# Performance work log

Measured on AMD Instinct MI355X. Metric: run time of the kernel, lower is better.

The kernel has to match this reference:

```python
import jax, jax.numpy as jnp
import numpy as np

IOU_THRESHOLD = 0.2


def setup_inputs() -> dict:
    key = jax.random.key(0)
    k1, k2, k3 = jax.random.split(key, 3)
    S, Q, X, Y, Z = 3, 64, 128, 128, 32
    C = 21  # 20 semantic classes + no-object
    voxel_logits = jax.random.normal(k1, (S, Q, X, Y, Z), dtype=jnp.float32)
    query_logits = jax.random.normal(k2, (S, 1, Q, C), dtype=jnp.float32)
    sem_prob_dense = jax.random.uniform(k3, (C, X, Y, Z), dtype=jnp.float32)
    return {"voxel_logits": voxel_logits, "query_logits": query_logits,
            "sem_prob_dense": sem_prob_dense}


def reference(voxel_logits, query_logits, sem_prob_dense):
    # voxel_logits: [S, Q, X, Y, Z], query_logits: [S, B, Q, C],
    # sem_prob_dense: [C_sem, X, Y, Z]
    S, Q, X, Y, Z = voxel_logits.shape
    N = X * Y * Z
    voxel_probs = jax.nn.sigmoid(voxel_logits).reshape(S, Q, N)   # MinkowskiSigmoid
    query_probs = jax.nn.softmax(query_logits, axis=-1)           # [S, B, Q, C]

    anchor_v = voxel_probs[0]   # [Q, N]
    anchor_q = query_probs[0]   # [B, Q, C]
    ious = []
    for i in range(1, S):  # small fixed loop over subnets
        aux_v = voxel_probs[i]
        # hard masks for IoU matching (find_matching_indices_v2)
        ma = (anchor_v > 0.5).astype(jnp.float32)  # [Q, N]
        mb = (aux_v > 0.5).astype(jnp.float32)     # [Q, N]
        inter = jnp.einsum('qn,pn->qp', ma, mb)    # [Q, Q]
        union = ma.sum(1)[:, None] + mb.sum(1)[None, :] - inter
        iou = inter / jnp.maximum(union, 1.0)
        aux_idx = jnp.argmax(iou, axis=1)          # best aux query per anchor
        iou_a = jnp.max(iou, axis=1)               # [Q]
        matched = iou_a > IOU_THRESHOLD
        # running-average merge of matched queries, weight i : 1
        merged_q = (anchor_q * i + query_probs[i][:, aux_idx, :]) / (i + 1)
        anchor_q = jnp.where(matched[None, :, None], merged_q, anchor_q)
        merged_v = (anchor_v * i + aux_v[aux_idx]) / (i + 1)
        anchor_v = jnp.where(matched[:, None], merged_v, anchor_v)
        ious.append(iou_a)

    iou_mean = jnp.stack(ious, axis=0).mean(0)     # [Q]
    keep = (iou_mean > IOU_THRESHOLD).astype(anchor_v.dtype)
    # mask out voxels whose ensemble semantic class is empty (class 0)
    sem_class = jnp.argmax(sem_prob_dense, axis=0)           # [X, Y, Z]
    occ = (sem_class != 0).astype(anchor_v.dtype).reshape(N)
    out = anchor_v * keep[:, None] * occ[None, :]
    return out.reshape(Q, X, Y, Z)
```

## Files before the change

kernel.cpp:

```cpp
#include <hip/hip_runtime.h>
#include <math.h>

#define NVOX 524288
#define WPR  8192
#define QN   64
#define SN   3
#define CN   21

__device__ __forceinline__ float sigmoidf_(float x) {
    return 1.0f / (1.0f + expf(-x));
}

__global__ __launch_bounds__(256) void mask_kernel(
    const float* __restrict__ logits, unsigned long long* __restrict__ B) {
    int tid = threadIdx.x;
    int wave = tid >> 6, lane = tid & 63;
    int wbase = (blockIdx.x * 4 + wave) * 4;
#pragma unroll
    for (int k = 0; k < 4; ++k) {
        int wi = wbase + k;
        int r = wi >> 13;
        int w = wi & (WPR - 1);
        float x = logits[r * NVOX + (w << 6) + lane];
        unsigned long long m = __ballot(x > 0.0f);
        if (lane == 0) B[wi] = m;
    }
}

__global__ __launch_bounds__(256) void rowsum_kernel(
    const unsigned long long* __restrict__ B, unsigned int* __restrict__ cnt) {
    int r = blockIdx.x, tid = threadIdx.x;
    const unsigned long long* row = B + r * WPR;
    int s = 0;
    for (int w = tid; w < WPR; w += 256) s += __popcll(row[w]);
    for (int off = 32; off; off >>= 1) s += __shfl_down(s, off);
    __shared__ int red[4];
    if ((tid & 63) == 0) red[tid >> 6] = s;
    __syncthreads();
    if (tid == 0) cnt[r] = (unsigned)(red[0] + red[1] + red[2] + red[3]);
}

__global__ __launch_bounds__(256) void inter_kernel(
    const unsigned long long* __restrict__ Ba,
    const unsigned long long* __restrict__ Bb,
    unsigned int* __restrict__ inter) {
    int q0 = blockIdx.y * 4, p0 = blockIdx.x * 4;
    int tid = threadIdx.x;
    int acc[4][4] = {};
    for (int w = tid; w < WPR; w += 256) {
        unsigned long long a[4], b[4];
#pragma unroll
        for (int i = 0; i < 4; ++i) a[i] = Ba[(q0 + i) * WPR + w];
#pragma unroll
        for (int j = 0; j < 4; ++j) b[j] = Bb[(p0 + j) * WPR + w];
#pragma unroll
        for (int i = 0; i < 4; ++i)
#pragma unroll
            for (int j = 0; j < 4; ++j) acc[i][j] += __popcll(a[i] & b[j]);
    }
    __shared__ int red[16][4];
    int lane = tid & 63, wave = tid >> 6;
#pragma unroll
    for (int i = 0; i < 4; ++i)
#pragma unroll
        for (int j = 0; j < 4; ++j) {
            int v = acc[i][j];
            for (int off = 32; off; off >>= 1) v += __shfl_down(v, off);
            if (lane == 0) red[i * 4 + j][wave] = v;
        }
    __syncthreads();
    if (tid < 16) {
        int s = red[tid][0] + red[tid][1] + red[tid][2] + red[tid][3];
        inter[(q0 + (tid >> 2)) * QN + (p0 + (tid & 3))] = (unsigned)s;
    }
}

__global__ void finalize_kernel(
    const unsigned int* __restrict__ inter,
    const unsigned int* __restrict__ cnt_a,
    const unsigned int* __restrict__ cnt_b,
    int* __restrict__ idx, int* __restrict__ matched,
    float* __restrict__ iou_out,
    int stage2, const float* __restrict__ iou_prev, float* __restrict__ keep) {
    int q = threadIdx.x;
    if (q >= QN) return;
    float na = (float)cnt_a[q];
    float best = -1.0f;
    int bidx = 0;
    for (int p = 0; p < QN; ++p) {
        float fi = (float)inter[q * QN + p];
        float un = fmaxf(na + (float)cnt_b[p] - fi, 1.0f);
        float iou = fi / un;
        if (iou > best) { best = iou; bidx = p; }
    }
    idx[q] = bidx;
    iou_out[q] = best;
    matched[q] = (best > 0.2f) ? 1 : 0;
    if (stage2) keep[q] = (((iou_prev[q] + best) * 0.5f) > 0.2f) ? 1.0f : 0.0f;
}

__global__ __launch_bounds__(256) void mask2_kernel(
    const float* __restrict__ logits,
    const int* __restrict__ idx1, const int* __restrict__ m1,
    unsigned long long* __restrict__ B0p) {
    int tid = threadIdx.x;
    int wave = tid >> 6, lane = tid & 63;
    int wbase = (blockIdx.x * 4 + wave) * 4;
    int q = wbase >> 13;
    int m = m1[q], j = idx1[q];
    const float* L0 = logits;
    const float* L1 = logits + QN * NVOX;
#pragma unroll
    for (int k = 0; k < 4; ++k) {
        int wi = wbase + k;
        int w = wi & (WPR - 1);
        int n = (w << 6) + lane;
        float x0 = L0[q * NVOX + n];
        bool pred;
        if (m) {
            float s0 = sigmoidf_(x0);
            float s1 = sigmoidf_(L1[j * NVOX + n]);
            pred = (s0 + s1) > 1.0f;
        } else {
            pred = x0 > 0.0f;
        }
        unsigned long long mk = __ballot(pred);
        if (lane == 0) B0p[wi] = mk;
    }
}

__global__ __launch_bounds__(256) void final_kernel(
    const float* __restrict__ logits,
    const float* __restrict__ sem,
    const int* __restrict__ idx1_, const int* __restrict__ m1_,
    const int* __restrict__ idx2_, const int* __restrict__ m2_,
    const float* __restrict__ keep_,
    float* __restrict__ out) {
    __shared__ int sidx1[QN], sm1[QN], sidx2[QN], sm2[QN];
    __shared__ float skeep[QN];
    int tid = threadIdx.x;
    if (tid < QN) {
        sidx1[tid] = idx1_[tid]; sm1[tid] = m1_[tid];
        sidx2[tid] = idx2_[tid]; sm2[tid] = m2_[tid];
        skeep[tid] = keep_[tid];
    }
    __syncthreads();
    int n = blockIdx.x * 256 + tid;
    float s0c = sem[n];
    float mx = sem[NVOX + n];
#pragma unroll
    for (int c = 2; c < CN; ++c) mx = fmaxf(mx, sem[c * NVOX + n]);
    float occ = (mx > s0c) ? 1.0f : 0.0f;
    const float* L0 = logits;
    const float* L1 = logits + QN * NVOX;
    const float* L2 = logits + 2 * QN * NVOX;
    for (int q = 0; q < QN; ++q) {
        float a = sigmoidf_(L0[q * NVOX + n]);
        if (sm1[q]) {
            float s1 = sigmoidf_(L1[sidx1[q] * NVOX + n]);
            a = (a + s1) * 0.5f;
        }
        if (sm2[q]) {
            float s2 = sigmoidf_(L2[sidx2[q] * NVOX + n]);
            a = (a * 2.0f + s2) / 3.0f;
        }
        out[q * NVOX + n] = a * skeep[q] * occ;
    }
}

extern "C" void kernel_launch(void* const* d_in, const int* in_sizes, int n_in,
                              void* d_out, int out_size, void* d_ws, size_t ws_size,
                              hipStream_t stream) {
    const float* vox = (const float*)d_in[0];
    const float* sem = (const float*)d_in[2];
    float* out = (float*)d_out;

    char* p = (char*)d_ws;
    unsigned long long* Ball = (unsigned long long*)p;
    unsigned long long* B0  = Ball;
    unsigned long long* B1  = Ball + 1 * QN * WPR;
    unsigned long long* B2  = Ball + 2 * QN * WPR;
    unsigned long long* B0p = Ball + 3 * QN * WPR;
    unsigned int* inter1 = (unsigned int*)(p + 16u * 1024u * 1024u);
    unsigned int* inter2 = inter1 + QN * QN;
    unsigned int* cnt    = inter2 + QN * QN;
    int*   idx1 = (int*)(cnt + 256);
    int*   idx2 = idx1 + QN;
    int*   m1   = idx2 + QN;
    int*   m2   = m1 + QN;
    float* iou1 = (float*)(m2 + QN);
    float* iou2 = iou1 + QN;
    float* keep = iou2 + QN;
    (void)in_sizes; (void)n_in; (void)out_size; (void)ws_size;

    mask_kernel<<<(SN * QN * WPR) / 16, 256, 0, stream>>>(vox, Ball);
    rowsum_kernel<<<SN * QN, 256, 0, stream>>>(Ball, cnt);

    inter_kernel<<<dim3(16, 16), 256, 0, stream>>>(B0, B1, inter1);
    finalize_kernel<<<1, 64, 0, stream>>>(inter1, cnt, cnt + QN, idx1, m1, iou1,
                                          0, nullptr, nullptr);

    mask2_kernel<<<(QN * WPR) / 16, 256, 0, stream>>>(vox, idx1, m1, B0p);
    rowsum_kernel<<<QN, 256, 0, stream>>>(B0p, cnt + 3 * QN);
    inter_kernel<<<dim3(16, 16), 256, 0, stream>>>(B0p, B2, inter2);
    finalize_kernel<<<1, 64, 0, stream>>>(inter2, cnt + 3 * QN, cnt + 2 * QN,
                                          idx2, m2, iou2, 1, iou1, keep);

    final_kernel<<<NVOX / 256, 256, 0, stream>>>(vox, sem, idx1, m1, idx2, m2,
                                                 keep, out);
}
```

Measured before the change: 892.2 us.

## Vectorize all passes with float4, fuse mask+rowsum, precompute occupancy, skip unmatched rows

Rewrites most kernels around float4 loads. The bitmask pass now also produces per-block popcount partials, which removes the separate rowsum kernels. The second-stage mask kernel skips unmatched queries by reusing the stage-0 bitmask in place, and it uses the logit-sum sign test instead of two sigmoids. Occupancy is computed once into a workspace buffer rather than per final block. The final kernel splits queries across two grid rows and uses fast exp and reciprocal intrinsics. The fast sigmoid slightly changes numerics, and the bit layout within each 256-voxel segment is permuted consistently for all masks.

```diff
diff --git a/kernel.cpp b/kernel.cpp
--- a/kernel.cpp
+++ b/kernel.cpp
@@ -1,62 +1,87 @@
 #include <hip/hip_runtime.h>
-#include <math.h>
 
 #define NVOX 524288
+#define NV4  131072
 #define WPR  8192
 #define QN   64
 #define SN   3
 #define CN   21
 
-__device__ __forceinline__ float sigmoidf_(float x) {
-    return 1.0f / (1.0f + expf(-x));
-}
-
-__global__ __launch_bounds__(256) void mask_kernel(
-    const float* __restrict__ logits, unsigned long long* __restrict__ B) {
-    int tid = threadIdx.x;
-    int wave = tid >> 6, lane = tid & 63;
-    int wbase = (blockIdx.x * 4 + wave) * 4;
-#pragma unroll
-    for (int k = 0; k < 4; ++k) {
-        int wi = wbase + k;
-        int r = wi >> 13;
-        int w = wi & (WPR - 1);
-        float x = logits[r * NVOX + (w << 6) + lane];
-        unsigned long long m = __ballot(x > 0.0f);
-        if (lane == 0) B[wi] = m;
-    }
-}
-
-__global__ __launch_bounds__(256) void rowsum_kernel(
-    const unsigned long long* __restrict__ B, unsigned int* __restrict__ cnt) {
-    int r = blockIdx.x, tid = threadIdx.x;
-    const unsigned long long* row = B + r * WPR;
-    int s = 0;
-    for (int w = tid; w < WPR; w += 256) s += __popcll(row[w]);
-    for (int off = 32; off; off >>= 1) s += __shfl_down(s, off);
+typedef unsigned long long u64;
+
+__device__ __forceinline__ float fast_sigmoid(float x) {
+    return __builtin_amdgcn_rcpf(1.0f + __expf(-x));
+}
+
+__global__ __launch_bounds__(256) void mask_rowsum_kernel(
+    const float4* __restrict__ logits4, u64* __restrict__ B,
+    unsigned int* __restrict__ part) {
+    int r = blockIdx.x >> 3, c = blockIdx.x & 7;
+    int tid = threadIdx.x, lane = tid & 63, wave = tid >> 6;
+    const float4* row = logits4 + (size_t)r * NV4;
+    int base = c * (NV4 / 8);
+    int pcnt = 0;
+#pragma unroll 2
+    for (int it = 0; it < 64; ++it) {
+        int idx = base + it * 256 + tid;
+        float4 v = row[idx];
+        int nib = (v.x > 0.f ? 1 : 0) | (v.y > 0.f ? 2 : 0) |
+                  (v.z > 0.f ? 4 : 0) | (v.w > 0.f ? 8 : 0);
+        pcnt += __popc(nib);
+        u64 b0 = __ballot(nib & 1);
+        u64 b1 = __ballot(nib & 2);
+        u64 b2 = __ballot(nib & 4);
+        u64 b3 = __ballot(nib & 8);
+        if (lane == 0) {
+            int seg = idx >> 6;
+            ulonglong2* dst = (ulonglong2*)&B[(size_t)r * WPR + (size_t)seg * 4];
+            dst[0] = make_ulonglong2(b0, b1);
+            dst[1] = make_ulonglong2(b2, b3);
+        }
+    }
+    for (int off = 32; off; off >>= 1) pcnt += __shfl_down(pcnt, off);
     __shared__ int red[4];
-    if ((tid & 63) == 0) red[tid >> 6] = s;
-    __syncthreads();
-    if (tid == 0) cnt[r] = (unsigned)(red[0] + red[1] + red[2] + red[3]);
+    if (lane == 0) red[wave] = pcnt;
+    __syncthreads();
+    if (tid == 0) part[blockIdx.x] = (unsigned)(red[0] + red[1] + red[2] + red[3]);
+}
+
+__global__ __launch_bounds__(256) void occ_kernel(
+    const float4* __restrict__ sem4, float4* __restrict__ occ4) {
+    int n4 = blockIdx.x * 256 + threadIdx.x;
+    float4 s0 = sem4[n4];
+    float4 mx = sem4[NV4 + n4];
+#pragma unroll
+    for (int c = 2; c < CN; ++c) {
+        float4 s = sem4[(size_t)c * NV4 + n4];
+        mx.x = fmaxf(mx.x, s.x); mx.y = fmaxf(mx.y, s.y);
+        mx.z = fmaxf(mx.z, s.z); mx.w = fmaxf(mx.w, s.w);
+    }
+    float4 o;
+    o.x = (mx.x > s0.x) ? 1.f : 0.f; o.y = (mx.y > s0.y) ? 1.f : 0.f;
+    o.z = (mx.z > s0.z) ? 1.f : 0.f; o.w = (mx.w > s0.w) ? 1.f : 0.f;
+    occ4[n4] = o;
 }
 
 __global__ __launch_bounds__(256) void inter_kernel(
-    const unsigned long long* __restrict__ Ba,
-    const unsigned long long* __restrict__ Bb,
+    const u64* __restrict__ Ba, const u64* __restrict__ Bb,
     unsigned int* __restrict__ inter) {
     int q0 = blockIdx.y * 4, p0 = blockIdx.x * 4;
     int tid = threadIdx.x;
+    const ulonglong2* A2 = (const ulonglong2*)Ba;
+    const ulonglong2* B2 = (const ulonglong2*)Bb;
     int acc[4][4] = {};
-    for (int w = tid; w < WPR; w += 256) {
-        unsigned long long a[4], b[4];
-#pragma unroll
-        for (int i = 0; i < 4; ++i) a[i] = Ba[(q0 + i) * WPR + w];
-#pragma unroll
-        for (int j = 0; j < 4; ++j) b[j] = Bb[(p0 + j) * WPR + w];
+    for (int w = tid; w < WPR / 2; w += 256) {
+        ulonglong2 a[4], b[4];
+#pragma unroll
+        for (int i = 0; i < 4; ++i) a[i] = A2[(size_t)(q0 + i) * (WPR / 2) + w];
+#pragma unroll
+        for (int j = 0; j < 4; ++j) b[j] = B2[(size_t)(p0 + j) * (WPR / 2) + w];
 #pragma unroll
         for (int i = 0; i < 4; ++i)
 #pragma unroll
-            for (int j = 0; j < 4; ++j) acc[i][j] += __popcll(a[i] & b[j]);
+            for (int j = 0; j < 4; ++j)
+                acc[i][j] += __popcll(a[i].x & b[j].x) + __popcll(a[i].y & b[j].y);
     }
     __shared__ int red[16][4];
     int lane = tid & 63, wave = tid >> 6;
@@ -77,19 +102,28 @@
 
 __global__ void finalize_kernel(
     const unsigned int* __restrict__ inter,
-    const unsigned int* __restrict__ cnt_a,
-    const unsigned int* __restrict__ cnt_b,
-    int* __restrict__ idx, int* __restrict__ matched,
-    float* __restrict__ iou_out,
+    const unsigned int* __restrict__ pa,
+    const unsigned int* __restrict__ pa_alt, const int* __restrict__ sel,
+    const unsigned int* __restrict__ pb,
+    int* __restrict__ idx, int* __restrict__ matched, float* __restrict__ iou_out,
     int stage2, const float* __restrict__ iou_prev, float* __restrict__ keep) {
+    __shared__ float nb[QN];
     int q = threadIdx.x;
-    if (q >= QN) return;
-    float na = (float)cnt_a[q];
+    unsigned sb = 0;
+#pragma unroll
+    for (int k = 0; k < 8; ++k) sb += pb[q * 8 + k];
+    nb[q] = (float)sb;
+    __syncthreads();
+    const unsigned int* pr = (sel && !sel[q]) ? pa_alt : pa;
+    unsigned sa = 0;
+#pragma unroll
+    for (int k = 0; k < 8; ++k) sa += pr[q * 8 + k];
+    float na = (float)sa;
     float best = -1.0f;
     int bidx = 0;
     for (int p = 0; p < QN; ++p) {
         float fi = (float)inter[q * QN + p];
-        float un = fmaxf(na + (float)cnt_b[p] - fi, 1.0f);
+        float un = fmaxf(na + nb[p] - fi, 1.0f);
         float iou = fi / un;
         if (iou > best) { best = iou; bidx = p; }
     }
@@ -100,112 +134,131 @@
 }
 
 __global__ __launch_bounds__(256) void mask2_kernel(
-    const float* __restrict__ logits,
+    const float4* __restrict__ logits4,
     const int* __restrict__ idx1, const int* __restrict__ m1,
-    unsigned long long* __restrict__ B0p) {
-    int tid = threadIdx.x;
-    int wave = tid >> 6, lane = tid & 63;
-    int wbase = (blockIdx.x * 4 + wave) * 4;
-    int q = wbase >> 13;
-    int m = m1[q], j = idx1[q];
-    const float* L0 = logits;
-    const float* L1 = logits + QN * NVOX;
-#pragma unroll
-    for (int k = 0; k < 4; ++k) {
-        int wi = wbase + k;
-        int w = wi & (WPR - 1);
-        int n = (w << 6) + lane;
-        float x0 = L0[q * NVOX + n];
-        bool pred;
-        if (m) {
-            float s0 = sigmoidf_(x0);
-            float s1 = sigmoidf_(L1[j * NVOX + n]);
-            pred = (s0 + s1) > 1.0f;
-        } else {
-            pred = x0 > 0.0f;
-        }
-        unsigned long long mk = __ballot(pred);
-        if (lane == 0) B0p[wi] = mk;
-    }
+    u64* __restrict__ B0p, unsigned int* __restrict__ partP) {
+    int q = blockIdx.x >> 3, c = blockIdx.x & 7;
+    if (!m1[q]) return;
+    int tid = threadIdx.x, lane = tid & 63, wave = tid >> 6;
+    const float4* r0 = logits4 + (size_t)q * NV4;
+    const float4* r1 = logits4 + (size_t)(QN + idx1[q]) * NV4;
+    int base = c * (NV4 / 8);
+    int pcnt = 0;
+#pragma unroll 2
+    for (int it = 0; it < 64; ++it) {
+        int idx = base + it * 256 + tid;
+        float4 a = r0[idx];
+        float4 b = r1[idx];
+        int nib = (a.x + b.x > 0.f ? 1 : 0) | (a.y + b.y > 0.f ? 2 : 0) |
+                  (a.z + b.z > 0.f ? 4 : 0) | (a.w + b.w > 0.f ? 8 : 0);
+        pcnt += __popc(nib);
+        u64 b0 = __ballot(nib & 1);
+        u64 b1 = __ballot(nib & 2);
+        u64 b2 = __ballot(nib & 4);
+        u64 b3 = __ballot(nib & 8);
+        if (lane == 0) {
+            int seg = idx >> 6;
+            ulonglong2* dst = (ulonglong2*)&B0p[(size_t)q * WPR + (size_t)seg * 4];
+            dst[0] = make_ulonglong2(b0, b1);
+            dst[1] = make_ulonglong2(b2, b3);
+        }
+    }
+    for (int off = 32; off; off >>= 1) pcnt += __shfl_down(pcnt, off);
+    __shared__ int red[4];
+    if (lane == 0) red[wave] = pcnt;
+    __syncthreads();
+    if (tid == 0) partP[blockIdx.x] = (unsigned)(red[0] + red[1] + red[2] + red[3]);
 }
 
 __global__ __launch_bounds__(256) void final_kernel(
-    const float* __restrict__ logits,
-    const float* __restrict__ sem,
+    const float4* __restrict__ logits4, const float4* __restrict__ occ4,
     const int* __restrict__ idx1_, const int* __restrict__ m1_,
     const int* __restrict__ idx2_, const int* __restrict__ m2_,
-    const float* __restrict__ keep_,
-    float* __restrict__ out) {
-    __shared__ int sidx1[QN], sm1[QN], sidx2[QN], sm2[QN];
-    __shared__ float skeep[QN];
+    const float* __restrict__ keep_, float4* __restrict__ out4) {
+    __shared__ int sj1[32], sm1[32], sj2[32], sm2[32];
+    __shared__ float sk[32];
     int tid = threadIdx.x;
-    if (tid < QN) {
-        sidx1[tid] = idx1_[tid]; sm1[tid] = m1_[tid];
-        sidx2[tid] = idx2_[tid]; sm2[tid] = m2_[tid];
-        skeep[tid] = keep_[tid];
-    }
-    __syncthreads();
-    int n = blockIdx.x * 256 + tid;
-    float s0c = sem[n];
-    float mx = sem[NVOX + n];
-#pragma unroll
-    for (int c = 2; c < CN; ++c) mx = fmaxf(mx, sem[c * NVOX + n]);
-    float occ = (mx > s0c) ? 1.0f : 0.0f;
-    const float* L0 = logits;
-    const float* L1 = logits + QN * NVOX;
-    const float* L2 = logits + 2 * QN * NVOX;
-    for (int q = 0; q < QN; ++q) {
-        float a = sigmoidf_(L0[q * NVOX + n]);
-        if (sm1[q]) {
-            float s1 = sigmoidf_(L1[sidx1[q] * NVOX + n]);
-            a = (a + s1) * 0.5f;
-        }
-        if (sm2[q]) {
-            float s2 = sigmoidf_(L2[sidx2[q] * NVOX + n]);
-            a = (a * 2.0f + s2) / 3.0f;
-        }
-        out[q * NVOX + n] = a * skeep[q] * occ;
+    int qbase = blockIdx.y * 32;
+    if (tid < 32) {
+        sj1[tid] = idx1_[qbase + tid]; sm1[tid] = m1_[qbase + tid];
+        sj2[tid] = idx2_[qbase + tid]; sm2[tid] = m2_[qbase + tid];
+        sk[tid] = keep_[qbase + tid];
+    }
+    __syncthreads();
+    int n4 = blockIdx.x * 256 + tid;
+    float4 oc = occ4[n4];
+#pragma unroll 2
+    for (int qq = 0; qq < 32; ++qq) {
+        int q = qbase + qq;
+        bool m1 = sm1[qq] != 0, m2 = sm2[qq] != 0;
+        float4 l0 = logits4[(size_t)q * NV4 + n4];
+        float4 l1 = logits4[(size_t)(QN + sj1[qq]) * NV4 + n4];
+        float4 l2 = logits4[(size_t)(2 * QN + sj2[qq]) * NV4 + n4];
+        float a0 = fast_sigmoid(l0.x), a1 = fast_sigmoid(l0.y);
+        float a2 = fast_sigmoid(l0.z), a3 = fast_sigmoid(l0.w);
+        if (m1) {
+            a0 = (a0 + fast_sigmoid(l1.x)) * 0.5f;
+            a1 = (a1 + fast_sigmoid(l1.y)) * 0.5f;
+            a2 = (a2 + fast_sigmoid(l1.z)) * 0.5f;
+            a3 = (a3 + fast_sigmoid(l1.w)) * 0.5f;
+        }
+        if (m2) {
+            const float t = 1.0f / 3.0f;
+            a0 = (a0 * 2.f + fast_sigmoid(l2.x)) * t;
+            a1 = (a1 * 2.f + fast_sigmoid(l2.y)) * t;
+            a2 = (a2 * 2.f + fast_sigmoid(l2.z)) * t;
+            a3 = (a3 * 2.f + fast_sigmoid(l2.w)) * t;
+        }
+        float kq = sk[qq];
+        float4 o;
+        o.x = a0 * kq * oc.x; o.y = a1 * kq * oc.y;
+        o.z = a2 * kq * oc.z; o.w = a3 * kq * oc.w;
+        out4[(size_t)q * NV4 + n4] = o;
     }
 }
 
 extern "C" void kernel_launch(void* const* d_in, const int* in_sizes, int n_in,
                               void* d_out, int out_size, void* d_ws, size_t ws_size,
                               hipStream_t stream) {
-    const float* vox = (const float*)d_in[0];
-    const float* sem = (const float*)d_in[2];
-    float* out = (float*)d_out;
+    const float4* vox4 = (const float4*)d_in[0];
+    const float4* sem4 = (const float4*)d_in[2];
+    float4* out4 = (float4*)d_out;
+    (void)in_sizes; (void)n_in; (void)out_size; (void)ws_size; (void)d_in;
 
     char* p = (char*)d_ws;
-    unsigned long long* Ball = (unsigned long long*)p;
-    unsigned long long* B0  = Ball;
-    unsigned long long* B1  = Ball + 1 * QN * WPR;
-    unsigned long long* B2  = Ball + 2 * QN * WPR;
-    unsigned long long* B0p = Ball + 3 * QN * WPR;
-    unsigned int* inter1 = (unsigned int*)(p + 16u * 1024u * 1024u);
+    u64* Ball = (u64*)p;
+    u64* B0 = Ball;
+    u64* B1 = Ball + 1 * (size_t)QN * WPR;
+    u64* B2 = Ball + 2 * (size_t)QN * WPR;
+    char* p2 = p + 3ull * QN * WPR * 8;
+    float4* occ4 = (float4*)p2;
+    char* p3 = p2 + (size_t)NVOX * 4;
+    unsigned int* inter1 = (unsigned int*)p3;
     unsigned int* inter2 = inter1 + QN * QN;
-    unsigned int* cnt    = inter2 + QN * QN;
-    int*   idx1 = (int*)(cnt + 256);
-    int*   idx2 = idx1 + QN;
-    int*   m1   = idx2 + QN;
-    int*   m2   = m1 + QN;
+    unsigned int* partA  = inter2 + QN * QN;
+    unsigned int* partP  = partA + 192 * 8;
+    int* idx1 = (int*)(partP + 64 * 8);
+    int* idx2 = idx1 + QN;
+    int* m1   = idx2 + QN;
+    int* m2   = m1 + QN;
     float* iou1 = (float*)(m2 + QN);
     float* iou2 = iou1 + QN;
     float* keep = iou2 + QN;
-    (void)in_sizes; (void)n_in; (void)out_size; (void)ws_size;
-
-    mask_kernel<<<(SN * QN * WPR) / 16, 256, 0, stream>>>(vox, Ball);
-    rowsum_kernel<<<SN * QN, 256, 0, stream>>>(Ball, cnt);
+
+    mask_rowsum_kernel<<<SN * QN * 8, 256, 0, stream>>>(vox4, Ball, partA);
+    occ_kernel<<<NV4 / 256, 256, 0, stream>>>(sem4, occ4);
 
     inter_kernel<<<dim3(16, 16), 256, 0, stream>>>(B0, B1, inter1);
-    finalize_kernel<<<1, 64, 0, stream>>>(inter1, cnt, cnt + QN, idx1, m1, iou1,
+    finalize_kernel<<<1, 64, 0, stream>>>(inter1, partA, nullptr, nullptr,
+                                          partA + QN * 8, idx1, m1, iou1,
                                           0, nullptr, nullptr);
 
-    mask2_kernel<<<(QN * WPR) / 16, 256, 0, stream>>>(vox, idx1, m1, B0p);
-    rowsum_kernel<<<QN, 256, 0, stream>>>(B0p, cnt + 3 * QN);
-    inter_kernel<<<dim3(16, 16), 256, 0, stream>>>(B0p, B2, inter2);
-    finalize_kernel<<<1, 64, 0, stream>>>(inter2, cnt + 3 * QN, cnt + 2 * QN,
-                                          idx2, m2, iou2, 1, iou1, keep);
-
-    final_kernel<<<NVOX / 256, 256, 0, stream>>>(vox, sem, idx1, m1, idx2, m2,
-                                                 keep, out);
-}
+    mask2_kernel<<<QN * 8, 256, 0, stream>>>(vox4, idx1, m1, B0, partP);
+    inter_kernel<<<dim3(16, 16), 256, 0, stream>>>(B0, B2, inter2);
+    finalize_kernel<<<1, 64, 0, stream>>>(inter2, partP, partA, m1,
+                                          partA + 2 * QN * 8, idx2, m2, iou2,
+                                          1, iou1, keep);
+
+    final_kernel<<<dim3(NV4 / 256, 2), 256, 0, stream>>>(
+        vox4, occ4, idx1, m1, idx2, m2, keep, out4);
+}
```

Result: faster. 745.5 us (-16.4%).
